# Kernel optimization log

Hardware: AMD Instinct MI355X
Metric: run time of the kernel (lower is better)

Reference implementation:

```python
import math
import jax, jax.numpy as jnp
import numpy as np

EMB = 1024
HEADS = 16
HEAD_DIM = EMB // HEADS


def setup_inputs() -> dict:
    key = jax.random.key(0)
    ks = jax.random.split(key, 6)
    b, l = 4, 4096
    x = jax.random.normal(ks[0], (b, l, EMB), dtype=jnp.float32)
    # torch Linear weight shape (out, in); xavier_normal std = sqrt(2/(in+out))
    std = math.sqrt(2.0 / (EMB + EMB))
    Wq = jax.random.normal(ks[1], (EMB, EMB), dtype=jnp.float32) * std
    Wk = jax.random.normal(ks[2], (EMB, EMB), dtype=jnp.float32) * std
    Wv = jax.random.normal(ks[3], (EMB, EMB), dtype=jnp.float32) * std
    Wu = jax.random.normal(ks[4], (EMB, EMB), dtype=jnp.float32) * std
    Wo = jax.random.normal(ks[5], (EMB, EMB), dtype=jnp.float32) * std
    return {"x": x, "Wq": Wq, "Wk": Wk, "Wv": Wv, "Wu": Wu, "Wo": Wo}


def _srms_norm(x, eps=1e-12):
    # SRMSNorm over last dim with scale 1/sqrt(head_dims), computed in fp32
    dtype = x.dtype
    xf = x.astype(jnp.float32)
    scale = 1.0 / math.sqrt(x.shape[-1])
    n = jnp.linalg.norm(xf * scale, axis=-1, keepdims=True)
    return (xf / jnp.maximum(n, eps)).astype(dtype)


def reference(x, Wq, Wk, Wv, Wu, Wo):
    b, l, d = x.shape
    h, hd = HEADS, HEAD_DIM
    scale = math.sqrt(hd)

    def proj(W):
        return jnp.einsum('bld,ed->ble', x, W).reshape(b, l, h, hd).transpose(0, 2, 1, 3)

    q = jax.nn.relu(proj(Wq)) / scale        # (b,h,l,hd)
    k = jax.nn.relu(proj(Wk)) / scale
    v = proj(Wv)
    u = jax.nn.silu(proj(Wu))

    kv = jnp.einsum('bhlk,bhlv->bhkv', k, v)  # (b,h,hd,hd) state
    out = jnp.einsum('bhlk,bhkv->bhlv', q, kv)
    out = _srms_norm(out) * u
    out = out.transpose(0, 2, 1, 3).reshape(b, l, d)
    return jnp.einsum('bld,ed->ble', out, Wo)
```

## Files before the change

kernel.cpp:

```cpp
#include <hip/hip_runtime.h>

typedef _Float16 f16;
typedef _Float16 f16x4 __attribute__((ext_vector_type(4)));
typedef _Float16 f16x8 __attribute__((ext_vector_type(8)));
typedef float f32x4 __attribute__((ext_vector_type(4)));

#define EMB 1024
#define SEQL 4096
#define BATCH 4
#define NH 16
#define HD 64
#define BH 64
#define MROWS 16384
#define KVSPLIT 16

#define GLOAD_LDS(gp, lp) \
    __builtin_amdgcn_global_load_lds((const __attribute__((address_space(1))) void*)(gp), \
                                     (__attribute__((address_space(3))) void*)(lp), 16, 0, 0)

__global__ void cvt_kernel(const float* __restrict__ in, f16* __restrict__ out, int n4) {
    int i = blockIdx.x * blockDim.x + threadIdx.x;
    if (i < n4) {
        float4 v = ((const float4*)in)[i];
        f16x4 o = { (f16)v.x, (f16)v.y, (f16)v.z, (f16)v.w };
        ((f16x4*)out)[i] = o;
    }
}

struct WPtrs { const float* p[5]; };

__global__ void cvt_w_kernel(WPtrs wp, f16* __restrict__ out) {
    int i = blockIdx.x * blockDim.x + threadIdx.x;
    int wsel = blockIdx.y;
    const float4* src = (const float4*)wp.p[wsel];
    float4 v = src[i];
    f16x4 o = { (f16)v.x, (f16)v.y, (f16)v.z, (f16)v.w };
    ((f16x4*)(out + (size_t)wsel * EMB * EMB))[i] = o;
}

__global__ void zero_kernel(float4* __restrict__ p, int n4) {
    int i = blockIdx.x * blockDim.x + threadIdx.x;
    if (i < n4) p[i] = float4{0.f, 0.f, 0.f, 0.f};
}

template<int MODE>
__global__ __launch_bounds__(256) void gemm_kernel(
    const f16* __restrict__ A, const f16* __restrict__ Bt,
    void* __restrict__ Cv, int M, int N, int K)
{
    __shared__ f16 As[128 * 32];
    __shared__ f16 Bs[128 * 32];

    const int lane = threadIdx.x & 63;
    const int w    = threadIdx.x >> 6;
    const int rw   = lane & 15;
    const int quad = lane >> 4;
    const int m0 = blockIdx.y * 128;
    const int n0 = blockIdx.x * 128;
    const int mw = (w >> 1) * 64;
    const int nw = (w & 1) * 64;

    const int srow = lane >> 2;
    const int scol = (lane & 3) * 8;
    const f16* ag0 = A  + (size_t)(m0 + w * 16 + srow) * K + scol;
    const f16* ag1 = A  + (size_t)(m0 + 64 + w * 16 + srow) * K + scol;
    const f16* bg0 = Bt + (size_t)(n0 + w * 16 + srow) * K + scol;
    const f16* bg1 = Bt + (size_t)(n0 + 64 + w * 16 + srow) * K + scol;
    f16* la0 = &As[(w * 16) * 32];
    f16* la1 = &As[(64 + w * 16) * 32];
    f16* lb0 = &Bs[(w * 16) * 32];
    f16* lb1 = &Bs[(64 + w * 16) * 32];

    f32x4 acc[4][4] = {};

    for (int k0 = 0; k0 < K; k0 += 32) {
        __syncthreads();
        GLOAD_LDS(ag0 + k0, la0);
        GLOAD_LDS(ag1 + k0, la1);
        GLOAD_LDS(bg0 + k0, lb0);
        GLOAD_LDS(bg1 + k0, lb1);
        __syncthreads();

        f16x8 af[4], bf[4];
        #pragma unroll
        for (int i = 0; i < 4; i++)
            af[i] = *(const f16x8*)&As[(mw + 16 * i + rw) * 32 + quad * 8];
        #pragma unroll
        for (int j = 0; j < 4; j++)
            bf[j] = *(const f16x8*)&Bs[(nw + 16 * j + rw) * 32 + quad * 8];
        #pragma unroll
        for (int i = 0; i < 4; i++)
            #pragma unroll
            for (int j = 0; j < 4; j++)
                acc[i][j] = __builtin_amdgcn_mfma_f32_16x16x32_f16(af[i], bf[j], acc[i][j], 0, 0, 0);
    }

    #pragma unroll
    for (int i = 0; i < 4; i++) {
        #pragma unroll
        for (int j = 0; j < 4; j++) {
            #pragma unroll
            for (int r = 0; r < 4; r++) {
                int row = m0 + mw + 16 * i + quad * 4 + r;
                int col = n0 + nw + 16 * j + rw;
                float v = acc[i][j][r];
                if (MODE == 0) {
                    ((float*)Cv)[(size_t)row * N + col] = v;
                } else if (MODE == 3) {
                    int sel = col >> 10, e = col & 1023;
                    float vv = sel ? (v / (1.0f + __expf(-v))) : (fmaxf(v, 0.0f) * 0.125f);
                    int b = row >> 12, l = row & 4095, h = e >> 6, hd = e & 63;
                    ((f16*)Cv)[(size_t)sel * MROWS * EMB +
                               (((size_t)(b * 16 + h) * 4096 + l) << 6) + hd] = (f16)vv;
                } else {
                    int sel = row >> 10, e = row & 1023;
                    float vv = sel ? v : (fmaxf(v, 0.0f) * 0.125f);
                    int b = col >> 12, l = col & 4095;
                    ((f16*)Cv)[(size_t)sel * MROWS * EMB +
                               (((size_t)b * 1024 + e) << 12) + l] = (f16)vv;
                }
            }
        }
    }
}

__global__ __launch_bounds__(256) void kv_split_kernel(
    const f16* __restrict__ kT, const f16* __restrict__ vT, float* __restrict__ kv32)
{
    const int bh    = blockIdx.x;
    const int chunk = blockIdx.y;
    const int lane  = threadIdx.x & 63;
    const int w     = threadIdx.x >> 6;
    const int rw    = lane & 15;
    const int quad  = lane >> 4;
    const int lbase = chunk * (SEQL / KVSPLIT);

    const f16* kp = kT + (size_t)bh * HD * SEQL + (size_t)(w * 16 + rw) * SEQL + lbase + quad * 8;
    const f16* vp = vT + (size_t)bh * HD * SEQL + (size_t)rw * SEQL + lbase + quad * 8;

    f32x4 acc[4] = {};
    for (int k0 = 0; k0 < SEQL / KVSPLIT; k0 += 32) {
        f16x8 a = *(const f16x8*)(kp + k0);
        #pragma unroll
        for (int t = 0; t < 4; t++) {
            f16x8 b = *(const f16x8*)(vp + (size_t)16 * t * SEQL + k0);
            acc[t] = __builtin_amdgcn_mfma_f32_16x16x32_f16(a, b, acc[t], 0, 0, 0);
        }
    }
    float* out = kv32 + (size_t)bh * HD * HD;
    #pragma unroll
    for (int t = 0; t < 4; t++)
        #pragma unroll
        for (int r = 0; r < 4; r++)
            atomicAdd(&out[(w * 16 + quad * 4 + r) * 64 + t * 16 + rw], acc[t][r]);
}

__global__ __launch_bounds__(256) void ret_out_kernel(
    const f16* __restrict__ q, const f16* __restrict__ u,
    const float* __restrict__ kv32, f16* __restrict__ o)
{
    const int bh    = blockIdx.x;
    const int chunk = blockIdx.y;
    const int lane  = threadIdx.x & 63;
    const int w     = threadIdx.x >> 6;
    const int rw    = lane & 15;
    const int quad  = lane >> 4;

    const float* kvp = kv32 + (size_t)bh * 4096;
    f16x8 bf[2][4];
    #pragma unroll
    for (int s = 0; s < 2; s++)
        #pragma unroll
        for (int t = 0; t < 4; t++)
            #pragma unroll
            for (int j = 0; j < 8; j++)
                bf[s][t][j] = (f16)kvp[(s * 32 + quad * 8 + j) * 64 + t * 16 + rw];

    const f16* qp = q + (size_t)bh * SEQL * HD;
    const f16* up = u + (size_t)bh * SEQL * HD;
    const int b = bh >> 4, h = bh & 15;
    f16* op = o + (size_t)b * SEQL * EMB + h * 64;

    const int l_wave = chunk * 512 + w * 128;
    for (int s = 0; s < 8; s++) {
        const int l0 = l_wave + s * 16;
        f16x8 a0 = *(const f16x8*)(qp + (size_t)(l0 + rw) * 64 + quad * 8);
        f16x8 a1 = *(const f16x8*)(qp + (size_t)(l0 + rw) * 64 + 32 + quad * 8);
        f32x4 acc[4] = {};
        #pragma unroll
        for (int t = 0; t < 4; t++) {
            acc[t] = __builtin_amdgcn_mfma_f32_16x16x32_f16(a0, bf[0][t], acc[t], 0, 0, 0);
            acc[t] = __builtin_amdgcn_mfma_f32_16x16x32_f16(a1, bf[1][t], acc[t], 0, 0, 0);
        }
        float inv[4];
        #pragma unroll
        for (int r = 0; r < 4; r++) {
            float ss = acc[0][r] * acc[0][r] + acc[1][r] * acc[1][r]
                     + acc[2][r] * acc[2][r] + acc[3][r] * acc[3][r];
            #pragma unroll
            for (int msk = 1; msk < 16; msk <<= 1)
                ss += __shfl_xor(ss, msk, 16);
            inv[r] = 8.0f / fmaxf(sqrtf(ss), 8e-12f);
        }
        #pragma unroll
        for (int t = 0; t < 4; t++)
            #pragma unroll
            for (int r = 0; r < 4; r++) {
                int l = l0 + quad * 4 + r;
                int col = t * 16 + rw;
                float uval = (float)up[(size_t)l * 64 + col];
                op[(size_t)l * EMB + col] = (f16)(acc[t][r] * inv[r] * uval);
            }
    }
}

extern "C" void kernel_launch(void* const* d_in, const int* in_sizes, int n_in,
                              void* d_out, int out_size, void* d_ws, size_t ws_size,
                              hipStream_t stream)
{
    const float* x = (const float*)d_in[0];
    WPtrs wp;
    wp.p[0] = (const float*)d_in[1];
    wp.p[1] = (const float*)d_in[4];
    wp.p[2] = (const float*)d_in[2];
    wp.p[3] = (const float*)d_in[3];
    wp.p[4] = (const float*)d_in[5];

    char* ws = (char*)d_ws;
    size_t off = 0;
    f16* x16 = (f16*)(ws + off); off += (size_t)MROWS * EMB * 2;
    f16* w16 = (f16*)(ws + off); off += (size_t)5 * EMB * EMB * 2;
    f16* qb  = (f16*)(ws + off); off += (size_t)MROWS * EMB * 2;
    f16* ub  = (f16*)(ws + off); off += (size_t)MROWS * EMB * 2;
    f16* kTb = (f16*)(ws + off); off += (size_t)MROWS * EMB * 2;
    f16* vTb = (f16*)(ws + off); off += (size_t)MROWS * EMB * 2;
    float* kv32 = (float*)(ws + off); off += (size_t)BH * HD * HD * 4;
    f16* ob  = x16;
    (void)ub; (void)vTb;

    cvt_kernel<<<(MROWS * EMB / 4) / 256, 256, 0, stream>>>(x, x16, MROWS * EMB / 4);
    cvt_w_kernel<<<dim3((EMB * EMB / 4) / 256, 5), 256, 0, stream>>>(wp, w16);
    zero_kernel<<<(BH * HD * HD / 4 + 255) / 256, 256, 0, stream>>>((float4*)kv32, BH * HD * HD / 4);

    f16* Wqu = w16;
    f16* Wkv = w16 + (size_t)2 * EMB * EMB;
    f16* Wo  = w16 + (size_t)4 * EMB * EMB;

    dim3 blk(256);
    gemm_kernel<3><<<dim3(16, 128), blk, 0, stream>>>(x16, Wqu, qb, MROWS, 2 * EMB, EMB);
    gemm_kernel<4><<<dim3(128, 16), blk, 0, stream>>>(Wkv, x16, kTb, 2 * EMB, MROWS, EMB);

    kv_split_kernel<<<dim3(BH, KVSPLIT), blk, 0, stream>>>(kTb, vTb, kv32);
    ret_out_kernel<<<dim3(BH, 8), blk, 0, stream>>>(qb, ub, kv32, ob);

    gemm_kernel<0><<<dim3(8, 128), blk, 0, stream>>>(ob, Wo, d_out, MROWS, EMB, EMB);
}
```

Measured before the change: 449.7 us.

## Swizzle GEMM LDS tiles and transpose MFMA operands for vectorized epilogue stores

Applies an XOR swizzle to the 16-byte column chunks, both on the global-to-LDS load side and on the fragment-read side, so that LDS reads from the 16 rows in a quad spread across banks. MFMA operands are swapped so each lane holds four consecutive output columns. This lets the epilogue write float4 or f16x4 vectors instead of scalar stores. The change is meant to cut LDS bank conflicts and the number of store instructions in all three GEMM modes, at the cost of some extra index arithmetic.

```diff
diff --git a/kernel.cpp b/kernel.cpp
--- a/kernel.cpp
+++ b/kernel.cpp
@@ -61,7 +61,7 @@
     const int nw = (w & 1) * 64;
 
     const int srow = lane >> 2;
-    const int scol = (lane & 3) * 8;
+    const int scol = (((lane & 3) ^ ((lane >> 3) & 3)) * 8);
     const f16* ag0 = A  + (size_t)(m0 + w * 16 + srow) * K + scol;
     const f16* ag1 = A  + (size_t)(m0 + 64 + w * 16 + srow) * K + scol;
     const f16* bg0 = Bt + (size_t)(n0 + w * 16 + srow) * K + scol;
@@ -71,6 +71,8 @@
     f16* lb0 = &Bs[(w * 16) * 32];
     f16* lb1 = &Bs[(64 + w * 16) * 32];
 
+    const int swz = (quad ^ ((rw >> 1) & 3)) * 8;
+
     f32x4 acc[4][4] = {};
 
     for (int k0 = 0; k0 < K; k0 += 32) {
@@ -84,41 +86,48 @@
         f16x8 af[4], bf[4];
         #pragma unroll
         for (int i = 0; i < 4; i++)
-            af[i] = *(const f16x8*)&As[(mw + 16 * i + rw) * 32 + quad * 8];
+            af[i] = *(const f16x8*)&As[(mw + 16 * i + rw) * 32 + swz];
         #pragma unroll
         for (int j = 0; j < 4; j++)
-            bf[j] = *(const f16x8*)&Bs[(nw + 16 * j + rw) * 32 + quad * 8];
+            bf[j] = *(const f16x8*)&Bs[(nw + 16 * j + rw) * 32 + swz];
         #pragma unroll
         for (int i = 0; i < 4; i++)
             #pragma unroll
             for (int j = 0; j < 4; j++)
-                acc[i][j] = __builtin_amdgcn_mfma_f32_16x16x32_f16(af[i], bf[j], acc[i][j], 0, 0, 0);
+                acc[i][j] = __builtin_amdgcn_mfma_f32_16x16x32_f16(bf[j], af[i], acc[i][j], 0, 0, 0);
     }
 
     #pragma unroll
     for (int i = 0; i < 4; i++) {
         #pragma unroll
         for (int j = 0; j < 4; j++) {
-            #pragma unroll
-            for (int r = 0; r < 4; r++) {
-                int row = m0 + mw + 16 * i + quad * 4 + r;
-                int col = n0 + nw + 16 * j + rw;
-                float v = acc[i][j][r];
-                if (MODE == 0) {
-                    ((float*)Cv)[(size_t)row * N + col] = v;
-                } else if (MODE == 3) {
-                    int sel = col >> 10, e = col & 1023;
-                    float vv = sel ? (v / (1.0f + __expf(-v))) : (fmaxf(v, 0.0f) * 0.125f);
-                    int b = row >> 12, l = row & 4095, h = e >> 6, hd = e & 63;
-                    ((f16*)Cv)[(size_t)sel * MROWS * EMB +
-                               (((size_t)(b * 16 + h) * 4096 + l) << 6) + hd] = (f16)vv;
-                } else {
-                    int sel = row >> 10, e = row & 1023;
-                    float vv = sel ? v : (fmaxf(v, 0.0f) * 0.125f);
-                    int b = col >> 12, l = col & 4095;
-                    ((f16*)Cv)[(size_t)sel * MROWS * EMB +
-                               (((size_t)b * 1024 + e) << 12) + l] = (f16)vv;
+            const int m_idx = m0 + mw + 16 * i + rw;
+            const int n_idx = n0 + nw + 16 * j + quad * 4;
+            if (MODE == 0) {
+                float4 vv = { acc[i][j][0], acc[i][j][1], acc[i][j][2], acc[i][j][3] };
+                *(float4*)&((float*)Cv)[(size_t)m_idx * N + n_idx] = vv;
+            } else if (MODE == 3) {
+                int sel = n_idx >> 10, e = n_idx & 1023;
+                int b = m_idx >> 12, l = m_idx & 4095, h = e >> 6, hd = e & 63;
+                f16x4 o;
+                #pragma unroll
+                for (int r = 0; r < 4; r++) {
+                    float v = acc[i][j][r];
+                    o[r] = (f16)(sel ? (v / (1.0f + __expf(-v))) : (fmaxf(v, 0.0f) * 0.125f));
                 }
+                *(f16x4*)&((f16*)Cv)[(size_t)sel * MROWS * EMB +
+                                     (((size_t)(b * 16 + h) * 4096 + l) << 6) + hd] = o;
+            } else {
+                int sel = m_idx >> 10, e = m_idx & 1023;
+                int b = n_idx >> 12, l = n_idx & 4095;
+                f16x4 o;
+                #pragma unroll
+                for (int r = 0; r < 4; r++) {
+                    float v = acc[i][j][r];
+                    o[r] = (f16)(sel ? v : (fmaxf(v, 0.0f) * 0.125f));
+                }
+                *(f16x4*)&((f16*)Cv)[(size_t)sel * MROWS * EMB +
+                                     (((size_t)b * 1024 + e) << 12) + l] = o;
             }
         }
     }
```

New measurement: 449.3 us. About the same (-0.1%).
